# Kernel tuning notes

Measured on AMD Instinct MI355X. Metric: run time of the kernel, lower is better.

## Reference

```python
import jax, jax.numpy as jnp
import numpy as np

C_IN = 128      # pair-rep channels (global_config['rep_2d']['num_c'])
C_ATT = 32      # attention_num_c
H = 4           # num_heads
LN_EPS = 1e-5


def setup_inputs() -> dict:
    key = jax.random.key(0)
    ks = jax.random.split(key, 8)
    B, N = 1, 256
    s = 0.02
    return {
        "x2d": jax.random.normal(ks[0], (B, N, N, C_IN), dtype=jnp.float32),
        "ln_g": jnp.ones((C_IN,), dtype=jnp.float32),
        "ln_b": jnp.zeros((C_IN,), dtype=jnp.float32),
        # nn.Linear(num_in_c, C_ATT*H*3, bias=False); stored as (in, out) for x @ W
        "W_qkv": jax.random.normal(ks[1], (C_IN, C_ATT * H * 3), dtype=jnp.float32) * s,
        "W_bias": jax.random.normal(ks[2], (C_IN, H), dtype=jnp.float32) * s,
        "W_gate": jax.random.normal(ks[3], (C_IN, C_ATT * H), dtype=jnp.float32) * s,
        "b_gate": jax.random.normal(ks[4], (C_ATT * H,), dtype=jnp.float32) * s,
        "W_out": jax.random.normal(ks[5], (C_ATT * H, C_IN), dtype=jnp.float32) * s,
        "b_out": jax.random.normal(ks[6], (C_IN,), dtype=jnp.float32) * s,
    }


def _layernorm(x, g, b):
    mu = jnp.mean(x, axis=-1, keepdims=True)
    var = jnp.mean(jnp.square(x - mu), axis=-1, keepdims=True)
    return (x - mu) * jax.lax.rsqrt(var + LN_EPS) * g + b


def reference(x2d, ln_g, ln_b, W_qkv, W_bias, W_gate, b_gate, W_out, b_out):
    B, N, _, _ = x2d.shape
    x = _layernorm(x2d, ln_g, ln_b)                       # (B,N,N,C_IN)

    # qkv: view(..., C_ATT, 3H) then chunk(3, dim=-1) -> each (..., C_ATT, H)
    qkv = (x @ W_qkv).reshape(B, N, N, C_ATT, 3 * H)
    q, k, v = qkv[..., :H], qkv[..., H:2 * H], qkv[..., 2 * H:]

    bias = x @ W_bias                                      # (B,I,J,H)
    g = jax.nn.sigmoid((x @ W_gate + b_gate).reshape(B, N, N, C_ATT, H))

    # torch: b.unsqueeze(1).transpose(2,3) -> (B,1,J,I,H); broadcast over i,
    # so w[b,i,j,k,h] += bias[b,k,j,h]
    b5 = jnp.transpose(bias, (0, 2, 1, 3))[:, None]        # (B,1,J,K,H) with K==I

    w = jnp.einsum('bijch,bikch->bijkh', q, k) / np.sqrt(C_ATT).astype(x.dtype) + b5
    w = jax.nn.softmax(w, axis=-2)                         # softmax over k

    out = jnp.einsum('bijkh,bikch->bijch', w, v) * g       # (B,I,J,C_ATT,H)
    out = out.reshape(B, N, N, C_ATT * H) @ W_out + b_out  # (B,N,N,C_IN)
    return out
```

## Files before the change

### kernel.cpp

```cpp
#include <hip/hip_runtime.h>

#define DEV __device__ __forceinline__

typedef unsigned short u16;
typedef __bf16 bf16x8 __attribute__((ext_vector_type(8)));
typedef u16 u16x4 __attribute__((ext_vector_type(4)));
typedef float fx4 __attribute__((ext_vector_type(4)));

#define NPIX 65536
#define OFF_WCAT  16777216
#define OFF_WOUT  16908288
#define OFF_Q     16941056
#define OFF_BIAS  67272704
#define OFF_GATE  68321280
#define TEN_ELEMS 8388608

DEV u16 f2bf(float f){
  unsigned u = __builtin_bit_cast(unsigned, f);
  u += 0x7fffu + ((u>>16)&1u);
  return (u16)(u>>16);
}
DEV float bf2f(u16 s){ return __builtin_bit_cast(float, ((unsigned)s)<<16); }

typedef __attribute__((address_space(1))) unsigned gas_t;
typedef __attribute__((address_space(3))) unsigned las_t;
DEV void gl16(const void* g, void* l){
  __builtin_amdgcn_global_load_lds((gas_t*)g, (las_t*)l, 16, 0, 0);
}

DEV int swz(int row, int cc){ return row*32 + (((cc + (row>>1))&3)<<3); }

__global__ __launch_bounds__(256) void k_prep(const float* __restrict__ Wqkv,
                                              const float* __restrict__ Wgate,
                                              const float* __restrict__ Wout,
                                              u16* __restrict__ wcat, u16* __restrict__ woutT){
  int idx = blockIdx.x*256 + threadIdx.x;
  int np = idx>>7, k = idx&127;
  int tt = np>>7, hh = (np>>5)&3, c = np&31;
  float v;
  if (tt < 3) v = Wqkv[k*384 + c*12 + tt*4 + hh];
  else        v = Wgate[k*128 + c*4 + hh];
  wcat[idx] = f2bf(v);
  if (idx < 16384){
    int n = idx>>7, kp = idx&127;
    int h2 = kp>>5, c2 = kp&31;
    woutT[idx] = f2bf(Wout[(c2*4 + h2)*128 + n]);
  }
}

__global__ __launch_bounds__(256) void k_ln(const float* __restrict__ x,
                                            const float* __restrict__ lng,
                                            const float* __restrict__ lnb,
                                            const float* __restrict__ Wb,
                                            u16* __restrict__ lnx, float* __restrict__ bias_s){
  int lane = threadIdx.x & 63;
  int wid  = (blockIdx.x*256 + threadIdx.x)>>6;
  int nw   = (gridDim.x*256)>>6;
  int c0 = lane<<1;
  float g0 = lng[c0], g1 = lng[c0+1], be0 = lnb[c0], be1 = lnb[c0+1];
  float4 wb0 = *(const float4*)(Wb + (c0<<2));
  float4 wb1 = *(const float4*)(Wb + (c0<<2) + 4);
  for (int p = wid; p < NPIX; p += nw){
    float2 xv = *(const float2*)(x + (((size_t)p)<<7) + c0);
    float s = xv.x + xv.y;
    float s2 = xv.x*xv.x + xv.y*xv.y;
    #pragma unroll
    for (int msk=32; msk>=1; msk>>=1){ s += __shfl_xor(s,msk); s2 += __shfl_xor(s2,msk); }
    float mu = s*(1.f/128.f);
    float var = s2*(1.f/128.f) - mu*mu;
    float rs = rsqrtf(var + 1e-5f);
    float y0 = (xv.x-mu)*rs*g0 + be0;
    float y1 = (xv.y-mu)*rs*g1 + be1;
    unsigned pk = (unsigned)f2bf(y0) | (((unsigned)f2bf(y1))<<16);
    *(unsigned*)(lnx + (((size_t)p)<<7) + c0) = pk;
    float d0 = y0*wb0.x + y1*wb1.x;
    float d1 = y0*wb0.y + y1*wb1.y;
    float d2 = y0*wb0.z + y1*wb1.z;
    float d3 = y0*wb0.w + y1*wb1.w;
    #pragma unroll
    for (int msk=32; msk>=1; msk>>=1){
      d0 += __shfl_xor(d0,msk); d1 += __shfl_xor(d1,msk);
      d2 += __shfl_xor(d2,msk); d3 += __shfl_xor(d3,msk);
    }
    if (lane==0){
      int pi = p>>8, pj = p&255;
      int o = (pj<<8) + pi;
      bias_s[o] = d0;
      bias_s[65536 + o] = d1;
      bias_s[131072 + o] = d2;
      bias_s[196608 + o] = d3;
    }
  }
}

__global__ __launch_bounds__(256,3) void k_qkv(const u16* __restrict__ lnx,
                                               const u16* __restrict__ wcat,
                                               const float* __restrict__ b_gate,
                                               u16* __restrict__ qkv, u16* __restrict__ gateb){
  __shared__ __align__(16) u16 As[4096];
  __shared__ __align__(16) u16 Bs[4096];
  __shared__ __align__(16) u16 Ep[64*132];
  int t = threadIdx.x, l = t&63, w = t>>6;
  int m0 = blockIdx.x<<7, n0 = blockIdx.y<<7;
  int tt2 = n0>>7;
  int wm = w>>1, wn = w&1;
  int rbase = (l>>4)<<2, cbase = l&15;
  fx4 acc[4][4] = {};
  for (int ks=0; ks<4; ++ks){
    int k0 = ks<<5;
    __syncthreads();
    #pragma unroll
    for (int s=0; s<2; ++s){
      int idx = (s<<8) + t;
      int row = idx>>2, ccL = idx&3;
      int ccG = (ccL - (row>>1)) & 3;
      gl16(lnx  + (size_t)(m0+row)*128 + k0 + (ccG<<3), As + (((s<<2)+w)<<9));
      gl16(wcat + (size_t)(n0+row)*128 + k0 + (ccG<<3), Bs + (((s<<2)+w)<<9));
    }
    asm volatile("s_waitcnt vmcnt(0)" ::: "memory");
    __syncthreads();
    bf16x8 a[4], b[4];
    #pragma unroll
    for (int mi=0; mi<4; ++mi)
      a[mi] = *(const bf16x8*)(As + swz((wm<<6)+(mi<<4)+cbase, l>>4));
    #pragma unroll
    for (int ni=0; ni<4; ++ni)
      b[ni] = *(const bf16x8*)(Bs + swz((wn<<6)+(ni<<4)+cbase, l>>4));
    #pragma unroll
    for (int mi=0; mi<4; ++mi)
      #pragma unroll
      for (int ni=0; ni<4; ++ni)
        acc[mi][ni] = __builtin_amdgcn_mfma_f32_16x16x32_bf16(a[mi], b[ni], acc[mi][ni], 0,0,0);
  }
  for (int half=0; half<2; ++half){
    __syncthreads();
    if (wm == half){
      #pragma unroll
      for (int mi=0; mi<4; ++mi)
        #pragma unroll
        for (int ni=0; ni<4; ++ni){
          int coln = (wn<<6) + (ni<<4) + cbase;
          if (tt2 == 3){
            float bg = b_gate[((coln&31)<<2) + (coln>>5)];
            #pragma unroll
            for (int r=0; r<4; ++r){
              int row = (mi<<4) + rbase + r;
              float v = acc[mi][ni][r] + bg;
              Ep[row*132 + coln] = f2bf(1.f/(1.f + __expf(-v)));
            }
          } else {
            #pragma unroll
            for (int r=0; r<4; ++r){
              int row = (mi<<4) + rbase + r;
              Ep[row*132 + coln] = f2bf(acc[mi][ni][r]);
            }
          }
        }
    }
    __syncthreads();
    int row = (w<<4) + (l>>2);
    int a4  = l&3;
    union V16 { u16x4 q[2]; bf16x8 o; };
    if (tt2 < 3){
      size_t base = (size_t)tt2*TEN_ELEMS + ((size_t)(m0>>8))*32768
                  + (size_t)((m0&255) + (half<<6) + row)*32;
      #pragma unroll
      for (int u=0; u<4; ++u){
        V16 v;
        v.q[0] = *(const u16x4*)(Ep + row*132 + (u<<5) + (a4<<3));
        v.q[1] = *(const u16x4*)(Ep + row*132 + (u<<5) + (a4<<3) + 4);
        *(bf16x8*)(qkv + base + (size_t)u*8192 + (a4<<3)) = v.o;
      }
    } else {
      size_t base = (size_t)(m0 + (half<<6) + row)*128;
      #pragma unroll
      for (int u=0; u<4; ++u){
        V16 v;
        v.q[0] = *(const u16x4*)(Ep + row*132 + (u<<5) + (a4<<3));
        v.q[1] = *(const u16x4*)(Ep + row*132 + (u<<5) + (a4<<3) + 4);
        *(bf16x8*)(gateb + base + (u<<5) + (a4<<3)) = v.o;
      }
    }
  }
}

__global__ __launch_bounds__(256,2) void k_attn(const u16* __restrict__ Qb,
                                                const u16* __restrict__ Kb,
                                                const u16* __restrict__ Vb,
                                                const float* __restrict__ bias_s,
                                                const u16* __restrict__ gateb,
                                                u16* __restrict__ Og){
  __shared__ __align__(16) u16 Ks[8192];
  __shared__ __align__(16) u16 Vs[8192];
  __shared__ __align__(16) u16 Pls[4][2176];
  int t = threadIdx.x, l = t&63, w = t>>6;
  int i = blockIdx.x>>2, h = blockIdx.x&3;
  size_t base2 = ((size_t)(i*4+h))<<13;
  #pragma unroll
  for (int s=0; s<4; ++s){
    int idx = (s<<8) + t;
    gl16(Kb + base2 + ((size_t)idx<<3), Ks + (((s<<2)+w)<<9));
    gl16(Vb + base2 + ((size_t)idx<<3), Vs + (((s<<2)+w)<<9));
  }
  asm volatile("s_waitcnt vmcnt(0)" ::: "memory");
  __syncthreads();
  int cbase = l&15, rbase = (l>>4)<<2;
  bf16x8 kf[16];
  #pragma unroll
  for (int f=0; f<16; ++f)
    kf[f] = *(const bf16x8*)(Ks + ((f<<4)+cbase)*32 + ((l>>4)<<3));
  bf16x8 vf[8][2];
  #pragma unroll
  for (int ks=0; ks<8; ++ks)
    #pragma unroll
    for (int cf=0; cf<2; ++cf){
      bf16x8 v;
      #pragma unroll
      for (int e=0; e<8; ++e)
        v[e] = __builtin_bit_cast(__bf16, Vs[((ks<<5) + ((l>>4)<<3) + e)*32 + (cf<<4) + cbase]);
      vf[ks][cf] = v;
    }
  u16* myP = &Pls[w][0];
  const float SCALE = 0.17677669529663687f;
  #pragma unroll 1
  for (int sj=0; sj<4; ++sj){
    int jloc = (w<<6) + (sj<<4);
    bf16x8 qf = *(const bf16x8*)(Qb + base2 + (size_t)(jloc + cbase)*32 + ((l>>4)<<3));
    fx4 sacc[16];
    #pragma unroll
    for (int f=0; f<16; ++f) sacc[f] = (fx4){0.f,0.f,0.f,0.f};
    #pragma unroll
    for (int f=0; f<16; ++f)
      sacc[f] = __builtin_amdgcn_mfma_f32_16x16x32_bf16(qf, kf[f], sacc[f], 0,0,0);
    const float* bp = bias_s + ((size_t)((h<<8) + jloc + rbase)<<8) + cbase;
    #pragma unroll
    for (int f=0; f<16; ++f)
      #pragma unroll
      for (int r=0; r<4; ++r)
        sacc[f][r] = sacc[f][r]*SCALE + bp[(r<<8) + (f<<4)];
    float mx[4], inv[4];
    #pragma unroll
    for (int r=0; r<4; ++r){
      float m = sacc[0][r];
      #pragma unroll
      for (int f=1; f<16; ++f) m = fmaxf(m, sacc[f][r]);
      m = fmaxf(m, __shfl_xor(m,1));
      m = fmaxf(m, __shfl_xor(m,2));
      m = fmaxf(m, __shfl_xor(m,4));
      m = fmaxf(m, __shfl_xor(m,8));
      mx[r] = m;
    }
    #pragma unroll
    for (int r=0; r<4; ++r){
      float sum = 0.f;
      #pragma unroll
      for (int f=0; f<16; ++f){ float p = __expf(sacc[f][r]-mx[r]); sacc[f][r] = p; sum += p; }
      sum += __shfl_xor(sum,1); sum += __shfl_xor(sum,2);
      sum += __shfl_xor(sum,4); sum += __shfl_xor(sum,8);
      inv[r] = 1.f/sum;
    }
    fx4 oacc[2] = {};
    #pragma unroll
    for (int half=0; half<2; ++half){
      #pragma unroll
      for (int f=0; f<8; ++f){
        int fk = (half<<3)+f;
        #pragma unroll
        for (int r=0; r<4; ++r)
          myP[(rbase+r)*136 + (f<<4) + cbase] = f2bf(sacc[fk][r]*inv[r]);
      }
      asm volatile("s_waitcnt lgkmcnt(0)" ::: "memory");
      #pragma unroll
      for (int k2=0; k2<4; ++k2){
        const bf16x8 pa = *(const bf16x8*)(myP + cbase*136 + (k2<<5) + ((l>>4)<<3));
        int ks = (half<<2)+k2;
        oacc[0] = __builtin_amdgcn_mfma_f32_16x16x32_bf16(pa, vf[ks][0], oacc[0], 0,0,0);
        oacc[1] = __builtin_amdgcn_mfma_f32_16x16x32_bf16(pa, vf[ks][1], oacc[1], 0,0,0);
      }
    }
    #pragma unroll
    for (int cf=0; cf<2; ++cf)
      #pragma unroll
      for (int r=0; r<4; ++r){
        int j = jloc + rbase + r;
        size_t pix = (((size_t)i)<<8) + j;
        int ch = (h<<5) + (cf<<4) + cbase;
        float gg = bf2f(gateb[(pix<<7) + ch]);
        Og[(pix<<7) + ch] = f2bf(oacc[cf][r]*gg);
      }
  }
}

__global__ __launch_bounds__(256,3) void k_out(const u16* __restrict__ og,
                                               const u16* __restrict__ wT,
                                               const float* __restrict__ bo,
                                               float* __restrict__ out){
  __shared__ __align__(16) u16 As[4096];
  __shared__ __align__(16) u16 Bs[4096];
  int t = threadIdx.x, l = t&63, w = t>>6;
  int m0 = blockIdx.x<<7;
  int wm = w>>1, wn = w&1;
  int rbase = (l>>4)<<2, cbase = l&15;
  fx4 acc[4][4] = {};
  for (int ks=0; ks<4; ++ks){
    int k0 = ks<<5;
    __syncthreads();
    #pragma unroll
    for (int s=0; s<2; ++s){
      int idx = (s<<8)+t, row = idx>>2, ccL = idx&3;
      int ccG = (ccL - (row>>1))&3;
      gl16(og + (size_t)(m0+row)*128 + k0 + (ccG<<3), As + (((s<<2)+w)<<9));
      gl16(wT + (size_t)row*128 + k0 + (ccG<<3), Bs + (((s<<2)+w)<<9));
    }
    asm volatile("s_waitcnt vmcnt(0)" ::: "memory");
    __syncthreads();
    bf16x8 a[4], b[4];
    #pragma unroll
    for (int mi=0; mi<4; ++mi)
      a[mi] = *(const bf16x8*)(As + swz((wm<<6)+(mi<<4)+cbase, l>>4));
    #pragma unroll
    for (int ni=0; ni<4; ++ni)
      b[ni] = *(const bf16x8*)(Bs + swz((wn<<6)+(ni<<4)+cbase, l>>4));
    #pragma unroll
    for (int mi=0; mi<4; ++mi)
      #pragma unroll
      for (int ni=0; ni<4; ++ni)
        acc[mi][ni] = __builtin_amdgcn_mfma_f32_16x16x32_bf16(a[mi], b[ni], acc[mi][ni], 0,0,0);
  }
  #pragma unroll
  for (int mi=0; mi<4; ++mi)
    #pragma unroll
    for (int ni=0; ni<4; ++ni){
      int n = (wn<<6)+(ni<<4)+cbase;
      float bn = bo[n];
      #pragma unroll
      for (int r=0; r<4; ++r){
        int m = m0 + (wm<<6)+(mi<<4)+rbase+r;
        out[(((size_t)m)<<7)+n] = acc[mi][ni][r] + bn;
      }
    }
}

extern "C" void kernel_launch(void* const* d_in, const int* in_sizes, int n_in,
                              void* d_out, int out_size, void* d_ws, size_t ws_size,
                              hipStream_t stream) {
  (void)in_sizes; (void)n_in; (void)out_size; (void)ws_size;
  const float* x2d    = (const float*)d_in[0];
  const float* ln_g   = (const float*)d_in[1];
  const float* ln_b   = (const float*)d_in[2];
  const float* W_qkv  = (const float*)d_in[3];
  const float* W_bias = (const float*)d_in[4];
  const float* W_gate = (const float*)d_in[5];
  const float* b_gate = (const float*)d_in[6];
  const float* W_out  = (const float*)d_in[7];
  const float* b_out  = (const float*)d_in[8];
  float* out = (float*)d_out;
  char* ws = (char*)d_ws;
  u16*   lnx    = (u16*)(ws);
  u16*   wcat   = (u16*)(ws + OFF_WCAT);
  u16*   woutT  = (u16*)(ws + OFF_WOUT);
  u16*   qkvb   = (u16*)(ws + OFF_Q);
  float* bias_s = (float*)(ws + OFF_BIAS);
  u16*   gateb  = (u16*)(ws + OFF_GATE);
  u16*   og     = lnx;

  hipLaunchKernelGGL(k_prep, dim3(256),      dim3(256), 0, stream, W_qkv, W_gate, W_out, wcat, woutT);
  hipLaunchKernelGGL(k_ln,   dim3(2048),     dim3(256), 0, stream, x2d, ln_g, ln_b, W_bias, lnx, bias_s);
  hipLaunchKernelGGL(k_qkv,  dim3(512,4),    dim3(256), 0, stream, lnx, wcat, b_gate, qkvb, gateb);
  hipLaunchKernelGGL(k_attn, dim3(1024),     dim3(256), 0, stream, qkvb, qkvb+TEN_ELEMS, qkvb+2*TEN_ELEMS, bias_s, gateb, og);
  hipLaunchKernelGGL(k_out,  dim3(512),      dim3(256), 0, stream, og, woutT, b_out, out);
}
```

Baseline: 128.8 us.

## Store V transposed from QKV epilogue and load attention fragments directly from global

The QKV GEMM epilogue now writes the V tensor channel-major (transposed) through a re-laid-out LDS staging buffer, so the attention kernel can load V fragments as contiguous 16-byte vectors straight from global memory instead of staging K/V in LDS and gathering V element-wise. The QK^T MFMA swaps operand order so each lane holds four consecutive keys, which allows float4 bias loads and reduces the softmax reductions to two cross-lane shuffles. The P tile is written once for all 256 keys with vector stores before the PV MFMAs, at the cost of a larger per-wave LDS buffer.

Result: slower. 171.1 us (+32.8%).

```diff
diff --git a/kernel.cpp b/kernel.cpp
--- a/kernel.cpp
+++ b/kernel.cpp
@@ -99,7 +99,7 @@
                                                u16* __restrict__ qkv, u16* __restrict__ gateb){
   __shared__ __align__(16) u16 As[4096];
   __shared__ __align__(16) u16 Bs[4096];
-  __shared__ __align__(16) u16 Ep[64*132];
+  __shared__ __align__(16) u16 Ep[9216];
   int t = threadIdx.x, l = t&63, w = t>>6;
   int m0 = blockIdx.x<<7, n0 = blockIdx.y<<7;
   int tt2 = n0>>7;
@@ -140,7 +140,12 @@
         #pragma unroll
         for (int ni=0; ni<4; ++ni){
           int coln = (wn<<6) + (ni<<4) + cbase;
-          if (tt2 == 3){
+          if (tt2 == 2){
+            u16x4 w4;
+            #pragma unroll
+            for (int r=0; r<4; ++r) w4[r] = f2bf(acc[mi][ni][r]);
+            *(u16x4*)(Ep + coln*72 + (mi<<4) + rbase) = w4;
+          } else if (tt2 == 3){
             float bg = b_gate[((coln&31)<<2) + (coln>>5)];
             #pragma unroll
             for (int r=0; r<4; ++r){
@@ -158,10 +163,21 @@
         }
     }
     __syncthreads();
-    int row = (w<<4) + (l>>2);
-    int a4  = l&3;
     union V16 { u16x4 q[2]; bf16x8 o; };
-    if (tt2 < 3){
+    if (tt2 == 2){
+      int col = t>>1;
+      int h2 = col>>5, c2 = col&31;
+      size_t base = 2*(size_t)TEN_ELEMS + ((size_t)(m0>>8))*32768
+                  + (size_t)h2*8192 + (size_t)c2*256
+                  + (m0&255) + (half<<6) + ((t&1)<<5);
+      #pragma unroll
+      for (int u=0; u<4; ++u){
+        bf16x8 v = *(const bf16x8*)(Ep + col*72 + ((t&1)<<5) + (u<<3));
+        *(bf16x8*)(qkv + base + (u<<3)) = v;
+      }
+    } else if (tt2 < 2){
+      int row = (w<<4) + (l>>2);
+      int a4  = l&3;
       size_t base = (size_t)tt2*TEN_ELEMS + ((size_t)(m0>>8))*32768
                   + (size_t)((m0&255) + (half<<6) + row)*32;
       #pragma unroll
@@ -172,6 +188,8 @@
         *(bf16x8*)(qkv + base + (size_t)u*8192 + (a4<<3)) = v.o;
       }
     } else {
+      int row = (w<<4) + (l>>2);
+      int a4  = l&3;
       size_t base = (size_t)(m0 + (half<<6) + row)*128;
       #pragma unroll
       for (int u=0; u<4; ++u){
@@ -186,103 +204,82 @@
 
 __global__ __launch_bounds__(256,2) void k_attn(const u16* __restrict__ Qb,
                                                 const u16* __restrict__ Kb,
-                                                const u16* __restrict__ Vb,
+                                                const u16* __restrict__ Vt,
                                                 const float* __restrict__ bias_s,
                                                 const u16* __restrict__ gateb,
                                                 u16* __restrict__ Og){
-  __shared__ __align__(16) u16 Ks[8192];
-  __shared__ __align__(16) u16 Vs[8192];
-  __shared__ __align__(16) u16 Pls[4][2176];
+  __shared__ __align__(16) u16 Pls[4][4224];
   int t = threadIdx.x, l = t&63, w = t>>6;
   int i = blockIdx.x>>2, h = blockIdx.x&3;
   size_t base2 = ((size_t)(i*4+h))<<13;
-  #pragma unroll
-  for (int s=0; s<4; ++s){
-    int idx = (s<<8) + t;
-    gl16(Kb + base2 + ((size_t)idx<<3), Ks + (((s<<2)+w)<<9));
-    gl16(Vb + base2 + ((size_t)idx<<3), Vs + (((s<<2)+w)<<9));
-  }
-  asm volatile("s_waitcnt vmcnt(0)" ::: "memory");
-  __syncthreads();
-  int cbase = l&15, rbase = (l>>4)<<2;
+  int cbase = l&15, g = l>>4;
   bf16x8 kf[16];
   #pragma unroll
   for (int f=0; f<16; ++f)
-    kf[f] = *(const bf16x8*)(Ks + ((f<<4)+cbase)*32 + ((l>>4)<<3));
+    kf[f] = *(const bf16x8*)(Kb + base2 + (size_t)(((f<<4)+cbase)<<5) + (g<<3));
   bf16x8 vf[8][2];
   #pragma unroll
   for (int ks=0; ks<8; ++ks)
     #pragma unroll
-    for (int cf=0; cf<2; ++cf){
-      bf16x8 v;
-      #pragma unroll
-      for (int e=0; e<8; ++e)
-        v[e] = __builtin_bit_cast(__bf16, Vs[((ks<<5) + ((l>>4)<<3) + e)*32 + (cf<<4) + cbase]);
-      vf[ks][cf] = v;
-    }
+    for (int cf=0; cf<2; ++cf)
+      vf[ks][cf] = *(const bf16x8*)(Vt + base2 + (size_t)(((cf<<4)+cbase)<<8) + (ks<<5) + (g<<3));
   u16* myP = &Pls[w][0];
   const float SCALE = 0.17677669529663687f;
   #pragma unroll 1
   for (int sj=0; sj<4; ++sj){
     int jloc = (w<<6) + (sj<<4);
-    bf16x8 qf = *(const bf16x8*)(Qb + base2 + (size_t)(jloc + cbase)*32 + ((l>>4)<<3));
+    bf16x8 qf = *(const bf16x8*)(Qb + base2 + (size_t)((jloc+cbase)<<5) + (g<<3));
     fx4 sacc[16];
     #pragma unroll
     for (int f=0; f<16; ++f) sacc[f] = (fx4){0.f,0.f,0.f,0.f};
     #pragma unroll
     for (int f=0; f<16; ++f)
-      sacc[f] = __builtin_amdgcn_mfma_f32_16x16x32_bf16(qf, kf[f], sacc[f], 0,0,0);
-    const float* bp = bias_s + ((size_t)((h<<8) + jloc + rbase)<<8) + cbase;
+      sacc[f] = __builtin_amdgcn_mfma_f32_16x16x32_bf16(kf[f], qf, sacc[f], 0,0,0);
+    const float* bp = bias_s + (((size_t)((h<<8) + jloc + cbase))<<8) + (g<<2);
+    #pragma unroll
+    for (int f=0; f<16; ++f){
+      float4 b4 = *(const float4*)(bp + (f<<4));
+      sacc[f][0] = sacc[f][0]*SCALE + b4.x;
+      sacc[f][1] = sacc[f][1]*SCALE + b4.y;
+      sacc[f][2] = sacc[f][2]*SCALE + b4.z;
+      sacc[f][3] = sacc[f][3]*SCALE + b4.w;
+    }
+    float m = sacc[0][0];
     #pragma unroll
     for (int f=0; f<16; ++f)
       #pragma unroll
-      for (int r=0; r<4; ++r)
-        sacc[f][r] = sacc[f][r]*SCALE + bp[(r<<8) + (f<<4)];
-    float mx[4], inv[4];
-    #pragma unroll
-    for (int r=0; r<4; ++r){
-      float m = sacc[0][r];
-      #pragma unroll
-      for (int f=1; f<16; ++f) m = fmaxf(m, sacc[f][r]);
-      m = fmaxf(m, __shfl_xor(m,1));
-      m = fmaxf(m, __shfl_xor(m,2));
-      m = fmaxf(m, __shfl_xor(m,4));
-      m = fmaxf(m, __shfl_xor(m,8));
-      mx[r] = m;
-    }
-    #pragma unroll
-    for (int r=0; r<4; ++r){
-      float sum = 0.f;
-      #pragma unroll
-      for (int f=0; f<16; ++f){ float p = __expf(sacc[f][r]-mx[r]); sacc[f][r] = p; sum += p; }
-      sum += __shfl_xor(sum,1); sum += __shfl_xor(sum,2);
-      sum += __shfl_xor(sum,4); sum += __shfl_xor(sum,8);
-      inv[r] = 1.f/sum;
-    }
+      for (int r=0; r<4; ++r) m = fmaxf(m, sacc[f][r]);
+    m = fmaxf(m, __shfl_xor(m,16));
+    m = fmaxf(m, __shfl_xor(m,32));
+    float s = 0.f;
+    #pragma unroll
+    for (int f=0; f<16; ++f)
+      #pragma unroll
+      for (int r=0; r<4; ++r){ float p = __expf(sacc[f][r]-m); sacc[f][r] = p; s += p; }
+    s += __shfl_xor(s,16);
+    s += __shfl_xor(s,32);
+    float inv = 1.f/s;
+    #pragma unroll
+    for (int f=0; f<16; ++f){
+      u16x4 w4;
+      #pragma unroll
+      for (int r=0; r<4; ++r) w4[r] = f2bf(sacc[f][r]*inv);
+      *(u16x4*)(myP + cbase*264 + (f<<4) + (g<<2)) = w4;
+    }
+    asm volatile("s_waitcnt lgkmcnt(0)" ::: "memory");
+    __builtin_amdgcn_sched_barrier(0);
     fx4 oacc[2] = {};
     #pragma unroll
-    for (int half=0; half<2; ++half){
-      #pragma unroll
-      for (int f=0; f<8; ++f){
-        int fk = (half<<3)+f;
-        #pragma unroll
-        for (int r=0; r<4; ++r)
-          myP[(rbase+r)*136 + (f<<4) + cbase] = f2bf(sacc[fk][r]*inv[r]);
-      }
-      asm volatile("s_waitcnt lgkmcnt(0)" ::: "memory");
-      #pragma unroll
-      for (int k2=0; k2<4; ++k2){
-        const bf16x8 pa = *(const bf16x8*)(myP + cbase*136 + (k2<<5) + ((l>>4)<<3));
-        int ks = (half<<2)+k2;
-        oacc[0] = __builtin_amdgcn_mfma_f32_16x16x32_bf16(pa, vf[ks][0], oacc[0], 0,0,0);
-        oacc[1] = __builtin_amdgcn_mfma_f32_16x16x32_bf16(pa, vf[ks][1], oacc[1], 0,0,0);
-      }
+    for (int ks=0; ks<8; ++ks){
+      const bf16x8 pa = *(const bf16x8*)(myP + cbase*264 + (ks<<5) + (g<<3));
+      oacc[0] = __builtin_amdgcn_mfma_f32_16x16x32_bf16(pa, vf[ks][0], oacc[0], 0,0,0);
+      oacc[1] = __builtin_amdgcn_mfma_f32_16x16x32_bf16(pa, vf[ks][1], oacc[1], 0,0,0);
     }
     #pragma unroll
     for (int cf=0; cf<2; ++cf)
       #pragma unroll
       for (int r=0; r<4; ++r){
-        int j = jloc + rbase + r;
+        int j = jloc + (g<<2) + r;
         size_t pix = (((size_t)i)<<8) + j;
         int ch = (h<<5) + (cf<<4) + cbase;
         float gg = bf2f(gateb[(pix<<7) + ch]);
```
